# Performance work log

Measured on AMD Instinct MI355X. Metric: run time of the kernel, lower is better.

The kernel has to match this reference:

```python
import jax, jax.numpy as jnp
import numpy as np

N = 100000   # nodes / embedding vocab
E = 1600000  # edges
D = 128      # feature dim
R = 7        # num relations
B = 4096     # matches
EPS = 1e-5


def setup_inputs() -> dict:
    key = jax.random.key(0)
    ks = jax.random.split(key, 12)
    s = 0.05
    return {
        "x": jnp.arange(N, dtype=jnp.int32),
        "edge_index": jax.random.randint(ks[0], (2, E), 0, N, dtype=jnp.int32),
        "edge_type": jax.random.randint(ks[1], (E,), 0, R, dtype=jnp.int32),
        "home": jax.random.randint(ks[2], (B,), 0, N, dtype=jnp.int32),
        "away": jax.random.randint(ks[3], (B,), 0, N, dtype=jnp.int32),
        "embed": jax.random.normal(ks[4], (N, D), jnp.float32) * s,
        "rel_w": jax.random.normal(ks[5], (3, R, D, D), jnp.float32) * s,
        "root_w": jax.random.normal(ks[6], (3, D, D), jnp.float32) * s,
        "conv_b": jnp.zeros((3, D), jnp.float32),
        "bn_gamma": jnp.ones((2, D), jnp.float32),
        "bn_beta": jnp.zeros((2, D), jnp.float32),
        "bn_mean": jnp.zeros((2, D), jnp.float32),
        "bn_var": jnp.ones((2, D), jnp.float32),
        "fc0_w": jax.random.normal(ks[7], (256, 2 * D), jnp.float32) * s,
        "fc0_b": jnp.zeros((256,), jnp.float32),
        "fc1_w": jax.random.normal(ks[8], (128, 256), jnp.float32) * s,
        "fc1_b": jnp.zeros((128,), jnp.float32),
        "fc2_w": jax.random.normal(ks[9], (3, 128), jnp.float32) * s,
        "fc2_b": jnp.zeros((3,), jnp.float32),
    }


def rgcn_conv(h, rel_w, root_w, bias, src, dst, seg):
    # PyG RGCNConv with aggr='mean': per-relation mean of source features,
    # aggregate-then-transform (valid since the relation transform is linear).
    n = h.shape[0]
    agg = jax.ops.segment_sum(h[src], seg, num_segments=n * R)      # [N*R, Din]
    cnt = jax.ops.segment_sum(jnp.ones((src.shape[0],), h.dtype), seg,
                              num_segments=n * R)                   # [N*R]
    agg = (agg / jnp.maximum(cnt, 1.0)[:, None]).reshape(n, R, -1)  # [N, R, Din]
    return jnp.einsum('nri,rio->no', agg, rel_w) + h @ root_w + bias


def reference(x, edge_index, edge_type, home, away, embed, rel_w, root_w, conv_b,
              bn_gamma, bn_beta, bn_mean, bn_var,
              fc0_w, fc0_b, fc1_w, fc1_b, fc2_w, fc2_b):
    src, dst = edge_index[0], edge_index[1]
    seg = dst.astype(jnp.int32) * R + edge_type  # combined (node, relation) id

    h = embed[x]  # [N, D]
    for l in range(2):
        h = rgcn_conv(h, rel_w[l], root_w[l], conv_b[l], src, dst, seg)
        h = (h - bn_mean[l]) * jax.lax.rsqrt(bn_var[l] + EPS) * bn_gamma[l] + bn_beta[l]
        h = jax.nn.relu(h)
    h = rgcn_conv(h, rel_w[2], root_w[2], conv_b[2], src, dst, seg)

    g = jnp.concatenate([h[home], h[away]], axis=1)  # [B, 2D]
    g = jax.nn.relu(g @ fc0_w.T + fc0_b)
    g = jax.nn.relu(g @ fc1_w.T + fc1_b)
    g = g @ fc2_w.T + fc2_b
    return jax.nn.log_softmax(g, axis=1)
```

## Files before the change

### kernel.cpp

```cpp
#include <hip/hip_runtime.h>
#include <hip/hip_bf16.h>

#define RR 7
#define EPSBN 1e-5f

typedef __attribute__((ext_vector_type(8))) __bf16 bf16x8;
typedef __attribute__((ext_vector_type(4))) float f32x4;
typedef __attribute__((ext_vector_type(2))) float f32x2;

__device__ __forceinline__ float uhi2f(unsigned int u) {
    union { unsigned int i; float f; } c; c.i = u; return c.f;
}
__device__ __forceinline__ unsigned short f2b(float f) {
    union { float f; unsigned int i; } c; c.f = f;
    unsigned int x = c.i;
    return (unsigned short)((x + 0x7fffu + ((x >> 16) & 1u)) >> 16);
}

__global__ void hist_k(const int* __restrict__ dst, const int* __restrict__ et,
                       int* __restrict__ cnt, int* __restrict__ rank, int ne) {
    int e = blockIdx.x * 256 + threadIdx.x;
    if (e < ne) rank[e] = atomicAdd(&cnt[dst[e] * RR + et[e]], 1);
}
__global__ void scan1_k(const int* __restrict__ cnt, int* __restrict__ bsum, int n) {
    __shared__ int sh[256];
    int base = blockIdx.x << 10;
    int s = 0;
    for (int i = threadIdx.x; i < 1024; i += 256) { int idx = base + i; if (idx < n) s += cnt[idx]; }
    sh[threadIdx.x] = s; __syncthreads();
    for (int off = 128; off > 0; off >>= 1) {
        if (threadIdx.x < off) sh[threadIdx.x] += sh[threadIdx.x + off];
        __syncthreads();
    }
    if (threadIdx.x == 0) bsum[blockIdx.x] = sh[0];
}
__global__ void scan2_k(int* __restrict__ bsum, int nb) {
    __shared__ int sh[256];
    int t = threadIdx.x;
    int v[4]; int loc = 0;
#pragma unroll
    for (int i = 0; i < 4; ++i) { int idx = t * 4 + i; v[i] = (idx < nb) ? bsum[idx] : 0; loc += v[i]; }
    sh[t] = loc; __syncthreads();
    for (int off = 1; off < 256; off <<= 1) {
        int x = (t >= off) ? sh[t - off] : 0;
        __syncthreads();
        sh[t] += x;
        __syncthreads();
    }
    int ex = (t > 0) ? sh[t - 1] : 0;
#pragma unroll
    for (int i = 0; i < 4; ++i) { int idx = t * 4 + i; if (idx < nb) { int vv = v[i]; bsum[idx] = ex; ex += vv; } }
}
__global__ void scan3_k(const int* __restrict__ cnt, const int* __restrict__ boff,
                        int* __restrict__ ptr, int n, int total) {
    __shared__ int sh[256];
    int t = threadIdx.x;
    int base = (blockIdx.x << 10) + (t << 2);
    int v[4]; int loc = 0;
#pragma unroll
    for (int i = 0; i < 4; ++i) { int idx = base + i; v[i] = (idx < n) ? cnt[idx] : 0; loc += v[i]; }
    sh[t] = loc; __syncthreads();
    for (int off = 1; off < 256; off <<= 1) {
        int x = (t >= off) ? sh[t - off] : 0;
        __syncthreads();
        sh[t] += x;
        __syncthreads();
    }
    int ex = boff[blockIdx.x] + ((t > 0) ? sh[t - 1] : 0);
#pragma unroll
    for (int i = 0; i < 4; ++i) {
        int idx = base + i;
        if (idx < n) { ptr[idx] = ex; ex += v[i]; }
    }
    if (blockIdx.x == 0 && t == 0) ptr[n] = total;
}
__global__ void scatter_k(const int* __restrict__ src, const int* __restrict__ dst,
                          const int* __restrict__ et, const int* __restrict__ rank,
                          const int* __restrict__ ptr, int* __restrict__ ssorted, int ne) {
    int e = blockIdx.x * 256 + threadIdx.x;
    if (e < ne) {
        int seg = dst[e] * RR + et[e];
        ssorted[ptr[seg] + rank[e]] = src[e];
    }
    if (blockIdx.x == 0 && threadIdx.x < 16) ssorted[ne + threadIdx.x] = 0;
}

__global__ __launch_bounds__(256) void prep_all_k(
    const float* __restrict__ rel_w, const float* __restrict__ root_w,
    unsigned short* __restrict__ wall,
    const int* __restrict__ x, const float* __restrict__ embed,
    unsigned short* __restrict__ h, int n, int nhb,
    const float* __restrict__ fc0w, const float* __restrict__ fc1w,
    float* __restrict__ w0t, float* __restrict__ w1t,
    const float* __restrict__ conv_b,
    const float* __restrict__ bn_g, const float* __restrict__ bn_b,
    const float* __restrict__ bn_m, const float* __restrict__ bn_v,
    float* __restrict__ AB)
{
    __shared__ unsigned short T[128][130];
    int b = blockIdx.x;
    int t = threadIdx.x;
    if (b < 24) {
        int l = b >> 3, kb = b & 7;
        const float* src = (kb < RR) ? rel_w + ((size_t)(l * RR + kb) << 14)
                                     : root_w + ((size_t)l << 14);
        for (int c = t; c < 4096; c += 256) {
            float4 f = *(const float4*)(src + (c << 2));
            int i = c >> 5, o = (c & 31) << 2;
            T[i][o] = f2b(f.x); T[i][o+1] = f2b(f.y); T[i][o+2] = f2b(f.z); T[i][o+3] = f2b(f.w);
        }
        __syncthreads();
        unsigned short* dst = wall + ((size_t)b << 14);
        for (int c = t; c < 2048; c += 256) {
            int frag = c >> 6;
            int lane = c & 63;
            int ks = frag >> 3, nt = frag & 7;
            int o = (nt << 4) + (lane & 15);
            int ib = (ks << 5) + ((lane >> 4) << 3);
            uint4 o4;
            o4.x = (unsigned)T[ib+0][o] | ((unsigned)T[ib+1][o] << 16);
            o4.y = (unsigned)T[ib+2][o] | ((unsigned)T[ib+3][o] << 16);
            o4.z = (unsigned)T[ib+4][o] | ((unsigned)T[ib+5][o] << 16);
            o4.w = (unsigned)T[ib+6][o] | ((unsigned)T[ib+7][o] << 16);
            *(uint4*)(dst + (c << 3)) = o4;
        }
    } else if (b < 24 + nhb) {
        int i = (b - 24) * 256 + t;
        if (i < n * 16) {
            int node = i >> 4, c8 = (i & 15) << 3;
            const float* e = embed + ((size_t)x[node] << 7) + c8;
            float4 f0 = *(const float4*)e;
            float4 f1 = *(const float4*)(e + 4);
            uint4 o4;
            o4.x = (unsigned)f2b(f0.x) | ((unsigned)f2b(f0.y) << 16);
            o4.y = (unsigned)f2b(f0.z) | ((unsigned)f2b(f0.w) << 16);
            o4.z = (unsigned)f2b(f1.x) | ((unsigned)f2b(f1.y) << 16);
            o4.w = (unsigned)f2b(f1.z) | ((unsigned)f2b(f1.w) << 16);
            *(uint4*)(h + ((size_t)node << 7) + c8) = o4;
        }
    } else if (b < 24 + nhb + 256) {
        int idx = ((b - 24 - nhb) << 8) + t;
        int o = idx & 255, i = idx >> 8;
        w0t[idx] = fc0w[o * 256 + i];
    } else if (b < 24 + nhb + 384) {
        int idx = ((b - 24 - nhb - 256) << 8) + t;
        int o = idx & 127, i = idx >> 7;
        w1t[idx] = fc1w[o * 256 + i];
    } else {
        for (int q = t; q < 384; q += 256) {
            int l = q >> 7, j = q & 127;
            float A = 1.f, Bv = conv_b[(l << 7) + j];
            if (l < 2) {
                float sc = bn_g[(l << 7) + j] * rsqrtf(bn_v[(l << 7) + j] + EPSBN);
                A = sc;
                Bv = Bv * sc + (bn_b[(l << 7) + j] - bn_m[(l << 7) + j] * sc);
            }
            AB[(l << 8) + j] = A;
            AB[(l << 8) + 128 + j] = Bv;
        }
    }
}

#define PAIRF(pw) ((f32x2){uhi2f((pw) << 16), uhi2f((pw) & 0xffff0000u)})
#define ACCP(b, u) { av2[(b)+0] += PAIRF((u).x); av2[(b)+1] += PAIRF((u).y); \
                     av2[(b)+2] += PAIRF((u).z); av2[(b)+3] += PAIRF((u).w); }
#define ACCW(b, u, wgt) { av2[(b)+0] += (f32x2){wgt,wgt} * PAIRF((u).x); \
                          av2[(b)+1] += (f32x2){wgt,wgt} * PAIRF((u).y); \
                          av2[(b)+2] += (f32x2){wgt,wgt} * PAIRF((u).z); \
                          av2[(b)+3] += (f32x2){wgt,wgt} * PAIRF((u).w); }
#define GATH(s) { const unsigned short* hp = h_in + ((size_t)(s) << 7) + (quad << 3); \
                  uint4 u0 = *(const uint4*)(hp);       uint4 u1 = *(const uint4*)(hp + 32); \
                  uint4 u2 = *(const uint4*)(hp + 64);  uint4 u3 = *(const uint4*)(hp + 96); \
                  ACCP(0, u0); ACCP(4, u1); ACCP(8, u2); ACCP(12, u3); }
#define LOADROW(a, b, c, d, s) { const unsigned short* hp = h_in + ((size_t)(s) << 7) + (quad << 3); \
                  (a) = *(const uint4*)(hp);      (b) = *(const uint4*)(hp + 32); \
                  (c) = *(const uint4*)(hp + 64); (d) = *(const uint4*)(hp + 96); }

__global__ __launch_bounds__(256, 3) void layer_k(
    const unsigned short* __restrict__ h_in,
    unsigned short* __restrict__ h_out,
    const unsigned short* __restrict__ wfrag,
    const float* __restrict__ AB,
    const int* __restrict__ seg_ptr, const int* __restrict__ src_sorted,
    const int* __restrict__ list_a, const int* __restrict__ list_b, int listB,
    int nout, int bnrelu)
{
    const int tid  = threadIdx.x;
    const int wave = tid >> 6;
    const int lane = tid & 63;
    const int n16  = lane & 15;
    const int quad = lane >> 4;
    const int row0 = blockIdx.x << 6;
    const int gidx = row0 + (wave << 4) + n16;
    const bool valid = gidx < nout;
    int gnode = 0;
    if (valid) {
        gnode = list_a ? (gidx < listB ? list_a[gidx] : list_b[gidx - listB]) : gidx;
    }

    int p[8];
    {
        int b = valid ? gnode * RR : 0;
#pragma unroll
        for (int i = 0; i < 8; ++i) p[i] = seg_ptr[b + i];
    }

    f32x4 acc[8];
#pragma unroll
    for (int i = 0; i < 8; ++i) acc[i] = (f32x4){0.f, 0.f, 0.f, 0.f};

    const unsigned short* wl = wfrag + (lane << 3);

#pragma unroll
    for (int kb = 0; kb < 8; ++kb) {
        f32x2 av2[16];
#pragma unroll
        for (int i = 0; i < 16; ++i) av2[i] = (f32x2){0.f, 0.f};
        float scale = 1.f;
        if (kb < RR) {
            int e0 = p[kb], e1 = p[kb + 1];
            int cnt = valid ? (e1 - e0) : 0;
            if (cnt > 0) scale = __builtin_amdgcn_rcpf((float)cnt);
            int cm = cnt - 1; if (cm < 0) cm = 0;
            int o1 = cm < 1 ? cm : 1;
            int o2 = cm < 2 ? cm : 2;
            int o3 = cm < 3 ? cm : 3;
            int s0 = src_sorted[e0];
            int s1 = src_sorted[e0 + o1];
            int s2 = src_sorted[e0 + o2];
            int s3 = src_sorted[e0 + o3];
            uint4 a0, a1, a2, a3, b0, b1, b2, b3, c0, c1, c2, c3, d0, d1, d2, d3;
            LOADROW(a0, a1, a2, a3, s0);
            LOADROW(b0, b1, b2, b3, s1);
            LOADROW(c0, c1, c2, c3, s2);
            LOADROW(d0, d1, d2, d3, s3);
            float q0 = cnt > 0 ? 1.f : 0.f;
            float q1 = cnt > 1 ? 1.f : 0.f;
            float q2 = cnt > 2 ? 1.f : 0.f;
            float q3 = cnt > 3 ? 1.f : 0.f;
            ACCW(0, a0, q0); ACCW(4, a1, q0); ACCW(8, a2, q0); ACCW(12, a3, q0);
            ACCW(0, b0, q1); ACCW(4, b1, q1); ACCW(8, b2, q1); ACCW(12, b3, q1);
            ACCW(0, c0, q2); ACCW(4, c1, q2); ACCW(8, c2, q2); ACCW(12, c3, q2);
            ACCW(0, d0, q3); ACCW(4, d1, q3); ACCW(8, d2, q3); ACCW(12, d3, q3);
            for (int e = e0 + 4; e < e0 + cnt; ++e) {
                int s = src_sorted[e];
                GATH(s);
            }
        } else {
            if (valid) GATH(gnode);
        }
        uint4 au[4];
#pragma unroll
        for (int ks = 0; ks < 4; ++ks) {
            unsigned pw[4];
#pragma unroll
            for (int m = 0; m < 4; ++m) {
                f32x2 q = av2[(ks << 2) + m] * scale;
                __hip_bfloat162 b2 = __float22bfloat162_rn(make_float2(q.x, q.y));
                unsigned uu; __builtin_memcpy(&uu, &b2, 4);
                pw[m] = uu;
            }
            au[ks].x = pw[0]; au[ks].y = pw[1]; au[ks].z = pw[2]; au[ks].w = pw[3];
        }
        const unsigned short* wk = wl + (kb << 14);
#pragma unroll
        for (int ks = 0; ks < 4; ++ks) {
            bf16x8 af;
            __builtin_memcpy(&af, &au[ks], 16);
#pragma unroll
            for (int nt = 0; nt < 8; ++nt) {
                bf16x8 bfr = *(const bf16x8*)(wk + (((ks << 3) + nt) << 9));
                acc[nt] = __builtin_amdgcn_mfma_f32_16x16x32_bf16(af, bfr, acc[nt], 0, 0, 0);
            }
        }
    }

#pragma unroll
    for (int nt = 0; nt < 8; ++nt) {
        int j = (nt << 4) + n16;
        float Aj = AB[j];
        float Bj = AB[128 + j];
#pragma unroll
        for (int r = 0; r < 4; ++r) {
            int orow = row0 + (wave << 4) + (quad << 2) + r;
            if (orow < nout) {
                float v = acc[nt][r] * Aj + Bj;
                if (bnrelu) v = fmaxf(v, 0.f);
                h_out[((size_t)orow << 7) + j] = f2b(v);
            }
        }
    }
}

__global__ __launch_bounds__(256) void mlp_k(
    const unsigned short* __restrict__ hC,
    const float* __restrict__ w0t, const float* __restrict__ bb0,
    const float* __restrict__ w1t, const float* __restrict__ bb1,
    const float* __restrict__ w2, const float* __restrict__ bb2,
    float* __restrict__ out, int Bn)
{
    __shared__ __attribute__((aligned(16))) float g0[16][256];
    __shared__ __attribute__((aligned(16))) float g1[16][256];
    __shared__ float lg[16][4];
    int t = threadIdx.x;
    {
        int row = t >> 4;
        int cseg = (t & 15) << 4;
        int gr = (blockIdx.x << 4) + row;
        int gc = (gr < Bn) ? gr : 0;
        const unsigned short* sp = (cseg < 128) ? (hC + ((size_t)gc << 7) + cseg)
                                                : (hC + ((size_t)(Bn + gc) << 7) + (cseg - 128));
#pragma unroll
        for (int c8 = 0; c8 < 2; ++c8) {
            uint4 v = *(const uint4*)(sp + (c8 << 3));
            int base = cseg + (c8 << 3);
            g0[row][base+0] = uhi2f(v.x << 16); g0[row][base+1] = uhi2f(v.x & 0xffff0000u);
            g0[row][base+2] = uhi2f(v.y << 16); g0[row][base+3] = uhi2f(v.y & 0xffff0000u);
            g0[row][base+4] = uhi2f(v.z << 16); g0[row][base+5] = uhi2f(v.z & 0xffff0000u);
            g0[row][base+6] = uhi2f(v.w << 16); g0[row][base+7] = uhi2f(v.w & 0xffff0000u);
        }
    }
    __syncthreads();
    {
        float acc[16];
#pragma unroll
        for (int r = 0; r < 16; ++r) acc[r] = 0.f;
#pragma unroll 4
        for (int i = 0; i < 256; ++i) {
            float w = w0t[(i << 8) + t];
#pragma unroll
            for (int r = 0; r < 16; ++r) acc[r] += w * g0[r][i];
        }
        float bb = bb0[t];
#pragma unroll
        for (int r = 0; r < 16; ++r) g1[r][t] = fmaxf(acc[r] + bb, 0.f);
    }
    __syncthreads();
    {
        int o = t & 127, rg = t >> 7;
        float acc[8];
#pragma unroll
        for (int r = 0; r < 8; ++r) acc[r] = 0.f;
#pragma unroll 4
        for (int i = 0; i < 256; ++i) {
            float w = w1t[(i << 7) + o];
#pragma unroll
            for (int r = 0; r < 8; ++r) acc[r] += w * g1[(rg << 3) + r][i];
        }
        float bb = bb1[o];
#pragma unroll
        for (int r = 0; r < 8; ++r) g0[(rg << 3) + r][o] = fmaxf(acc[r] + bb, 0.f);
    }
    __syncthreads();
    if (t < 48) {
        int row = t / 3, cls = t - row * 3;
        const float* wr = w2 + (cls << 7);
        float a = 0.f;
        for (int i = 0; i < 128; i += 4) {
            float4 w = *(const float4*)(wr + i);
            float4 g = *(const float4*)&g0[row][i];
            a += w.x * g.x + w.y * g.y + w.z * g.z + w.w * g.w;
        }
        lg[row][cls] = a + bb2[cls];
    }
    __syncthreads();
    if (t < 16) {
        int gr = (blockIdx.x << 4) + t;
        if (gr < Bn) {
            float l0 = lg[t][0], l1 = lg[t][1], l2 = lg[t][2];
            float m = fmaxf(l0, fmaxf(l1, l2));
            float lse = m + logf(expf(l0 - m) + expf(l1 - m) + expf(l2 - m));
            out[gr * 3 + 0] = l0 - lse;
            out[gr * 3 + 1] = l1 - lse;
            out[gr * 3 + 2] = l2 - lse;
        }
    }
}

extern "C" void kernel_launch(void* const* d_in, const int* in_sizes, int n_in,
                              void* d_out, int out_size, void* d_ws, size_t ws_size,
                              hipStream_t stream) {
    const int*   x      = (const int*)d_in[0];
    const int*   eidx   = (const int*)d_in[1];
    const int*   etype  = (const int*)d_in[2];
    const int*   home   = (const int*)d_in[3];
    const int*   away   = (const int*)d_in[4];
    const float* embed  = (const float*)d_in[5];
    const float* rel_w  = (const float*)d_in[6];
    const float* root_w = (const float*)d_in[7];
    const float* conv_b = (const float*)d_in[8];
    const float* bn_g   = (const float*)d_in[9];
    const float* bn_b   = (const float*)d_in[10];
    const float* bn_m   = (const float*)d_in[11];
    const float* bn_v   = (const float*)d_in[12];
    const float* fc0w   = (const float*)d_in[13];
    const float* fc0b   = (const float*)d_in[14];
    const float* fc1w   = (const float*)d_in[15];
    const float* fc1b   = (const float*)d_in[16];
    const float* fc2w   = (const float*)d_in[17];
    const float* fc2b   = (const float*)d_in[18];
    float* out = (float*)d_out;

    const int N_ = in_sizes[0];
    const int E_ = in_sizes[2];
    const int B_ = in_sizes[3];
    const int NS = N_ * RR;

    char* ws = (char*)d_ws;
    auto alloc = [&](size_t bytes) -> char* {
        char* p = ws;
        ws += (bytes + 255) & ~(size_t)255;
        return p;
    };
    int* ptr         = (int*)alloc((size_t)(NS + 1) * 4);
    int* cursor      = (int*)alloc((size_t)NS * 4);
    int* bsum        = (int*)alloc(4096);
    int* rank        = (int*)alloc((size_t)E_ * 4);
    int* src_sorted  = (int*)alloc((size_t)(E_ + 16) * 4);
    unsigned short* wall = (unsigned short*)alloc((size_t)3 * 8 * 16384 * 2);
    unsigned short* hA   = (unsigned short*)alloc((size_t)N_ * 128 * 2);
    unsigned short* hB   = (unsigned short*)alloc((size_t)N_ * 128 * 2);
    unsigned short* hC   = (unsigned short*)alloc((size_t)2 * B_ * 128 * 2);
    float* AB        = (float*)alloc(3 * 256 * 4);
    float* w0t       = (float*)alloc(65536 * 4);
    float* w1t       = (float*)alloc(32768 * 4);

    const int nb = (NS + 1023) / 1024;
    const int nhb = (N_ * 16 + 255) / 256;

    (void)hipMemsetAsync(cursor, 0, (size_t)NS * 4, stream);
    hist_k<<<(E_ + 255) / 256, 256, 0, stream>>>(eidx + E_, etype, cursor, rank, E_);
    scan1_k<<<nb, 256, 0, stream>>>(cursor, bsum, NS);
    scan2_k<<<1, 256, 0, stream>>>(bsum, nb);
    scan3_k<<<nb, 256, 0, stream>>>(cursor, bsum, ptr, NS, E_);
    scatter_k<<<(E_ + 255) / 256, 256, 0, stream>>>(eidx, eidx + E_, etype, rank, ptr,
                                                    src_sorted, E_);

    prep_all_k<<<24 + nhb + 384 + 1, 256, 0, stream>>>(
        rel_w, root_w, wall, x, embed, hA, N_, nhb,
        fc0w, fc1w, w0t, w1t, conv_b, bn_g, bn_b, bn_m, bn_v, AB);

    const int lgrid = (N_ + 63) / 64;
    layer_k<<<lgrid, 256, 0, stream>>>(hA, hB, wall + 0 * 8 * 16384, AB + 0,
                                       ptr, src_sorted, nullptr, nullptr, 0, N_, 1);
    layer_k<<<lgrid, 256, 0, stream>>>(hB, hA, wall + 1 * 8 * 16384, AB + 256,
                                       ptr, src_sorted, nullptr, nullptr, 0, N_, 1);
    const int n3 = 2 * B_;
    layer_k<<<(n3 + 63) / 64, 256, 0, stream>>>(hA, hC, wall + 2 * 8 * 16384, AB + 512,
                                                ptr, src_sorted, home, away, B_, n3, 0);

    mlp_k<<<(B_ + 15) / 16, 256, 0, stream>>>(hC, w0t, fc0b, w1t, fc1b,
                                              fc2w, fc2b, out, B_);
}
```

Before: 686.2 us.

## Compute layer-2 only for nodes feeding match endpoints; prefetch next segment indices

Adds mark and compact kernels that find the home/away nodes and their in-neighbours, and runs the second RGCN layer only on that compacted list, read from a device-side count, instead of on all nodes. Blocks past the live count exit early. The gather loop now prefetches the first four source indices of the next relation segment and branches on the count, replacing the masked fixed four-row loads. Occupancy is raised to 4 blocks per CU. The cost is extra small kernels, a memset and unordered compaction via atomics, and the full-size layer-2 grid still launches.

```diff
diff --git a/kernel.cpp b/kernel.cpp
--- a/kernel.cpp
+++ b/kernel.cpp
@@ -83,6 +83,22 @@
         ssorted[ptr[seg] + rank[e]] = src[e];
     }
     if (blockIdx.x == 0 && threadIdx.x < 16) ssorted[ne + threadIdx.x] = 0;
+}
+
+__global__ void mark_k(const int* __restrict__ home, const int* __restrict__ away,
+                       const int* __restrict__ ptr, const int* __restrict__ ssorted,
+                       int* __restrict__ mark, int Bn) {
+    int i = blockIdx.x * 256 + threadIdx.x;
+    if (i >= 2 * Bn) return;
+    int node = (i < Bn) ? home[i] : away[i - Bn];
+    mark[node] = 1;
+    int e0 = ptr[node * RR], e1 = ptr[node * RR + RR];
+    for (int e = e0; e < e1; ++e) mark[ssorted[e]] = 1;
+}
+__global__ void compact_k(const int* __restrict__ mark, int* __restrict__ list,
+                          int* __restrict__ count, int n) {
+    int i = blockIdx.x * 256 + threadIdx.x;
+    if (i < n && mark[i]) { int p = atomicAdd(count, 1); list[p] = i; }
 }
 
 __global__ __launch_bounds__(256) void prep_all_k(
@@ -164,26 +180,20 @@
 #define PAIRF(pw) ((f32x2){uhi2f((pw) << 16), uhi2f((pw) & 0xffff0000u)})
 #define ACCP(b, u) { av2[(b)+0] += PAIRF((u).x); av2[(b)+1] += PAIRF((u).y); \
                      av2[(b)+2] += PAIRF((u).z); av2[(b)+3] += PAIRF((u).w); }
-#define ACCW(b, u, wgt) { av2[(b)+0] += (f32x2){wgt,wgt} * PAIRF((u).x); \
-                          av2[(b)+1] += (f32x2){wgt,wgt} * PAIRF((u).y); \
-                          av2[(b)+2] += (f32x2){wgt,wgt} * PAIRF((u).z); \
-                          av2[(b)+3] += (f32x2){wgt,wgt} * PAIRF((u).w); }
 #define GATH(s) { const unsigned short* hp = h_in + ((size_t)(s) << 7) + (quad << 3); \
                   uint4 u0 = *(const uint4*)(hp);       uint4 u1 = *(const uint4*)(hp + 32); \
                   uint4 u2 = *(const uint4*)(hp + 64);  uint4 u3 = *(const uint4*)(hp + 96); \
                   ACCP(0, u0); ACCP(4, u1); ACCP(8, u2); ACCP(12, u3); }
-#define LOADROW(a, b, c, d, s) { const unsigned short* hp = h_in + ((size_t)(s) << 7) + (quad << 3); \
-                  (a) = *(const uint4*)(hp);      (b) = *(const uint4*)(hp + 32); \
-                  (c) = *(const uint4*)(hp + 64); (d) = *(const uint4*)(hp + 96); }
-
-__global__ __launch_bounds__(256, 3) void layer_k(
+
+__global__ __launch_bounds__(256, 4) void layer_k(
     const unsigned short* __restrict__ h_in,
     unsigned short* __restrict__ h_out,
     const unsigned short* __restrict__ wfrag,
     const float* __restrict__ AB,
     const int* __restrict__ seg_ptr, const int* __restrict__ src_sorted,
     const int* __restrict__ list_a, const int* __restrict__ list_b, int listB,
-    int nout, int bnrelu)
+    const int* __restrict__ nout_dev,
+    int nout, int bnrelu, int by_node)
 {
     const int tid  = threadIdx.x;
     const int wave = tid >> 6;
@@ -191,6 +201,8 @@
     const int n16  = lane & 15;
     const int quad = lane >> 4;
     const int row0 = blockIdx.x << 6;
+    if (nout_dev) nout = *nout_dev;
+    if (row0 >= nout) return;
     const int gidx = row0 + (wave << 4) + n16;
     const bool valid = gidx < nout;
     int gnode = 0;
@@ -209,6 +221,10 @@
 #pragma unroll
     for (int i = 0; i < 8; ++i) acc[i] = (f32x4){0.f, 0.f, 0.f, 0.f};
 
+    int sv0, sv1, sv2, sv3;
+    { int e0 = p[0]; sv0 = src_sorted[e0]; sv1 = src_sorted[e0+1];
+      sv2 = src_sorted[e0+2]; sv3 = src_sorted[e0+3]; }
+
     const unsigned short* wl = wfrag + (lane << 3);
 
 #pragma unroll
@@ -217,34 +233,25 @@
 #pragma unroll
         for (int i = 0; i < 16; ++i) av2[i] = (f32x2){0.f, 0.f};
         float scale = 1.f;
+        int nv0 = 0, nv1 = 0, nv2 = 0, nv3 = 0;
         if (kb < RR) {
-            int e0 = p[kb], e1 = p[kb + 1];
-            int cnt = valid ? (e1 - e0) : 0;
-            if (cnt > 0) scale = __builtin_amdgcn_rcpf((float)cnt);
-            int cm = cnt - 1; if (cm < 0) cm = 0;
-            int o1 = cm < 1 ? cm : 1;
-            int o2 = cm < 2 ? cm : 2;
-            int o3 = cm < 3 ? cm : 3;
-            int s0 = src_sorted[e0];
-            int s1 = src_sorted[e0 + o1];
-            int s2 = src_sorted[e0 + o2];
-            int s3 = src_sorted[e0 + o3];
-            uint4 a0, a1, a2, a3, b0, b1, b2, b3, c0, c1, c2, c3, d0, d1, d2, d3;
-            LOADROW(a0, a1, a2, a3, s0);
-            LOADROW(b0, b1, b2, b3, s1);
-            LOADROW(c0, c1, c2, c3, s2);
-            LOADROW(d0, d1, d2, d3, s3);
-            float q0 = cnt > 0 ? 1.f : 0.f;
-            float q1 = cnt > 1 ? 1.f : 0.f;
-            float q2 = cnt > 2 ? 1.f : 0.f;
-            float q3 = cnt > 3 ? 1.f : 0.f;
-            ACCW(0, a0, q0); ACCW(4, a1, q0); ACCW(8, a2, q0); ACCW(12, a3, q0);
-            ACCW(0, b0, q1); ACCW(4, b1, q1); ACCW(8, b2, q1); ACCW(12, b3, q1);
-            ACCW(0, c0, q2); ACCW(4, c1, q2); ACCW(8, c2, q2); ACCW(12, c3, q2);
-            ACCW(0, d0, q3); ACCW(4, d1, q3); ACCW(8, d2, q3); ACCW(12, d3, q3);
-            for (int e = e0 + 4; e < e0 + cnt; ++e) {
-                int s = src_sorted[e];
-                GATH(s);
+            if (kb < RR - 1) {
+                int en = p[kb + 1];
+                nv0 = src_sorted[en]; nv1 = src_sorted[en+1];
+                nv2 = src_sorted[en+2]; nv3 = src_sorted[en+3];
+            }
+            if (valid) {
+                int e0 = p[kb], e1 = p[kb + 1];
+                int cnt = e1 - e0;
+                if (cnt > 0) scale = __builtin_amdgcn_rcpf((float)cnt);
+                if (cnt > 0) GATH(sv0);
+                if (cnt > 1) GATH(sv1);
+                if (cnt > 2) GATH(sv2);
+                if (cnt > 3) GATH(sv3);
+                for (int e = e0 + 4; e < e1; ++e) {
+                    int s = src_sorted[e];
+                    GATH(s);
+                }
             }
         } else {
             if (valid) GATH(gnode);
@@ -273,8 +280,17 @@
                 acc[nt] = __builtin_amdgcn_mfma_f32_16x16x32_bf16(af, bfr, acc[nt], 0, 0, 0);
             }
         }
-    }
-
+        sv0 = nv0; sv1 = nv1; sv2 = nv2; sv3 = nv3;
+    }
+
+    int orow[4];
+#pragma unroll
+    for (int r = 0; r < 4; ++r) {
+        int ri = row0 + (wave << 4) + (quad << 2) + r;
+        if (ri < nout) {
+            orow[r] = by_node ? (ri < listB ? list_a[ri] : list_b[ri - listB]) : ri;
+        } else orow[r] = -1;
+    }
 #pragma unroll
     for (int nt = 0; nt < 8; ++nt) {
         int j = (nt << 4) + n16;
@@ -282,11 +298,10 @@
         float Bj = AB[128 + j];
 #pragma unroll
         for (int r = 0; r < 4; ++r) {
-            int orow = row0 + (wave << 4) + (quad << 2) + r;
-            if (orow < nout) {
+            if (orow[r] >= 0) {
                 float v = acc[nt][r] * Aj + Bj;
                 if (bnrelu) v = fmaxf(v, 0.f);
-                h_out[((size_t)orow << 7) + j] = f2b(v);
+                h_out[((size_t)orow[r] << 7) + j] = f2b(v);
             }
         }
     }
@@ -417,6 +432,8 @@
     int* bsum        = (int*)alloc(4096);
     int* rank        = (int*)alloc((size_t)E_ * 4);
     int* src_sorted  = (int*)alloc((size_t)(E_ + 16) * 4);
+    int* mark        = (int*)alloc((size_t)(N_ + 1) * 4);
+    int* flist       = (int*)alloc((size_t)N_ * 4);
     unsigned short* wall = (unsigned short*)alloc((size_t)3 * 8 * 16384 * 2);
     unsigned short* hA   = (unsigned short*)alloc((size_t)N_ * 128 * 2);
     unsigned short* hB   = (unsigned short*)alloc((size_t)N_ * 128 * 2);
@@ -424,11 +441,13 @@
     float* AB        = (float*)alloc(3 * 256 * 4);
     float* w0t       = (float*)alloc(65536 * 4);
     float* w1t       = (float*)alloc(32768 * 4);
+    int* fcount      = mark + N_;
 
     const int nb = (NS + 1023) / 1024;
     const int nhb = (N_ * 16 + 255) / 256;
 
     (void)hipMemsetAsync(cursor, 0, (size_t)NS * 4, stream);
+    (void)hipMemsetAsync(mark, 0, (size_t)(N_ + 1) * 4, stream);
     hist_k<<<(E_ + 255) / 256, 256, 0, stream>>>(eidx + E_, etype, cursor, rank, E_);
     scan1_k<<<nb, 256, 0, stream>>>(cursor, bsum, NS);
     scan2_k<<<1, 256, 0, stream>>>(bsum, nb);
@@ -436,18 +455,24 @@
     scatter_k<<<(E_ + 255) / 256, 256, 0, stream>>>(eidx, eidx + E_, etype, rank, ptr,
                                                     src_sorted, E_);
 
+    mark_k<<<(2 * B_ + 255) / 256, 256, 0, stream>>>(home, away, ptr, src_sorted, mark, B_);
+    compact_k<<<(N_ + 255) / 256, 256, 0, stream>>>(mark, flist, fcount, N_);
+
     prep_all_k<<<24 + nhb + 384 + 1, 256, 0, stream>>>(
         rel_w, root_w, wall, x, embed, hA, N_, nhb,
         fc0w, fc1w, w0t, w1t, conv_b, bn_g, bn_b, bn_m, bn_v, AB);
 
     const int lgrid = (N_ + 63) / 64;
     layer_k<<<lgrid, 256, 0, stream>>>(hA, hB, wall + 0 * 8 * 16384, AB + 0,
-                                       ptr, src_sorted, nullptr, nullptr, 0, N_, 1);
+                                       ptr, src_sorted, nullptr, nullptr, 0,
+                                       nullptr, N_, 1, 0);
     layer_k<<<lgrid, 256, 0, stream>>>(hB, hA, wall + 1 * 8 * 16384, AB + 256,
-                                       ptr, src_sorted, nullptr, nullptr, 0, N_, 1);
+                                       ptr, src_sorted, flist, flist, N_,
+                                       fcount, N_, 1, 1);
     const int n3 = 2 * B_;
     layer_k<<<(n3 + 63) / 64, 256, 0, stream>>>(hA, hC, wall + 2 * 8 * 16384, AB + 512,
-                                                ptr, src_sorted, home, away, B_, n3, 0);
+                                                ptr, src_sorted, home, away, B_,
+                                                nullptr, n3, 0, 0);
 
     mlp_k<<<(B_ + 15) / 16, 256, 0, stream>>>(hC, w0t, fc0b, w1t, fc1b,
                                               fc2w, fc2b, out, B_);
```

Measured after the change: 633.0 us. 7.8% less time.
